# Optimization experiments

Hardware: AMD Instinct MI355X
Metric: run time of the kernel (lower is better)

## Reference

```python
import jax, jax.numpy as jnp
import numpy as np

GAMMA = 0.01
INFER_STEP = 5


def softor(x, axis, gamma=GAMMA):
    # gamma * logsumexp(x / gamma) along `axis`, rescaled by global max if it exceeds 1
    y = gamma * jax.nn.logsumexp(x / gamma, axis=axis)
    mx = jnp.max(y)
    return jnp.where(mx > 1.0, y / mx, y)


def setup_inputs() -> dict:
    key = jax.random.key(0)
    k1, k2, k3 = jax.random.split(key, 3)
    B, G, C, S, L, m = 32, 2048, 16, 8, 3, 16
    x = jax.random.uniform(k1, (B, G), dtype=jnp.float32)          # valuation vector in [0,1]
    W = jax.random.normal(k2, (m, C), dtype=jnp.float32)           # clause-assignment weights
    I = jax.random.randint(k3, (C, G, S, L), 0, G)                 # index tensor into atom axis
    return {"x": x, "W": W, "I": I}


def reference(x, W, I):
    # x: [B,G] valuations; W: [m,C]; I: [C,G,S,L] int indices into G
    def r(V):
        # all C clause functions at once: gather V along atom axis using I
        gathered = V[:, I]                      # [B,C,G,S,L]
        body = jnp.prod(gathered, axis=-1)      # conjunction over body literals -> [B,C,G,S]
        Cv = softor(body, axis=-1)              # softor over substitutions -> [B,C,G]
        Ws = jax.nn.softmax(W, axis=1)          # [m,C]
        H = jnp.einsum('mc,bcg->mbg', Ws, Cv)   # weighted clause mix -> [m,B,G]
        return softor(H, axis=0)                # softor over m heads -> [B,G]

    R = x
    for _ in range(INFER_STEP):
        R = softor(jnp.stack([R, r(R)], axis=1), axis=1)  # amalgamate old and new facts
    return R
```

## Files before the change

kernel.cpp:

```cpp
#include <hip/hip_runtime.h>

#define GAMMA 0.01f
#define B 32
#define G 2048
#define C 16
#define S 8
#define L 3
#define M 16
#define NBLK 256
#define NTHR 256

#define K_EXP 144.26950408889634f
#define K_LOG 0.006931471805599453f

#define SCOPE __HIP_MEMORY_SCOPE_AGENT

__device__ __forceinline__ unsigned ald(const unsigned* p) {
    return __hip_atomic_load(p, __ATOMIC_RELAXED, SCOPE);
}
__device__ __forceinline__ void ast(unsigned* p, unsigned v) {
    __hip_atomic_store(p, v, __ATOMIC_RELAXED, SCOPE);
}
__device__ __forceinline__ float aldf(const float* p) {
    return __hip_atomic_load(p, __ATOMIC_RELAXED, SCOPE);
}
__device__ __forceinline__ void astf(float* p, float v) {
    __hip_atomic_store(p, v, __ATOMIC_RELAXED, SCOPE);
}

__device__ __forceinline__ float waveMax(float v) {
#pragma unroll
    for (int off = 32; off > 0; off >>= 1)
        v = fmaxf(v, __shfl_xor(v, off, 64));
    return v;
}

__device__ __forceinline__ float blockMaxBcast(float v, float* scratch) {
    float wm = waveMax(v);
    __syncthreads();
    if ((threadIdx.x & 63) == 0) scratch[threadIdx.x >> 6] = wm;
    __syncthreads();
    return fmaxf(fmaxf(scratch[0], scratch[1]), fmaxf(scratch[2], scratch[3]));
}

__device__ __forceinline__ void blockMaxOut(float v, float* scratch, float* dst) {
    float wm = waveMax(v);
    __syncthreads();
    if ((threadIdx.x & 63) == 0) scratch[threadIdx.x >> 6] = wm;
    __syncthreads();
    if (threadIdx.x == 0)
        astf(&dst[blockIdx.x],
             fmaxf(fmaxf(scratch[0], scratch[1]), fmaxf(scratch[2], scratch[3])));
}

__device__ __forceinline__ void gridBarrier(unsigned* slots, unsigned* gen,
                                            unsigned* rgen, int bid, unsigned ep) {
    __syncthreads();
    const int t = threadIdx.x;
    if (bid == 0) {
        if (t > 0) {
            int guard = 0;
            while (ald(&slots[t * 32]) < ep && ++guard < (1 << 17)) {}
        }
        __syncthreads();
        if (t == 0) {
            asm volatile("s_waitcnt vmcnt(0) lgkmcnt(0)" ::: "memory");
            ast(gen, ep);
        }
    } else {
        if (t == 0) {
            asm volatile("s_waitcnt vmcnt(0) lgkmcnt(0)" ::: "memory");
            ast(&slots[bid * 32], ep);
            int guard = 0;
            if (bid <= 16) {
                while (ald(gen) < ep && ++guard < (1 << 17)) {}
                ast(&rgen[bid * 32], ep);
            } else {
                const int r = 1 + (bid & 15);
                while (ald(&rgen[r * 32]) < ep && ++guard < (1 << 17)) {}
            }
        }
        __syncthreads();
    }
}

extern "C" __global__ __launch_bounds__(256) void kmain(
    const float* __restrict__ x, const float* __restrict__ W,
    const int* __restrict__ I,
    unsigned* __restrict__ slots, unsigned* __restrict__ gen,
    unsigned* __restrict__ rgen, unsigned* __restrict__ Ipk,
    float* __restrict__ Pm1, float* __restrict__ Pm2, float* __restrict__ Pm3,
    float* __restrict__ Ry, float* __restrict__ out)
{
    __shared__ __align__(16) float Vrow[G];
    __shared__ float WsL[C * M];
    __shared__ float scratch[4];

    const int t = threadIdx.x;
    const int bid = blockIdx.x;
    const int b = bid & 31;
    const int gt = bid >> 5;
    const int g = (gt << 8) + t;
    const int i = b * G + g;
    unsigned ep = 0;

    {
        const int m = t >> 4, c = t & 15;
        float rmax = -INFINITY;
#pragma unroll
        for (int j = 0; j < C; j++) rmax = fmaxf(rmax, W[m * C + j]);
        float rsum = 0.f;
#pragma unroll
        for (int j = 0; j < C; j++) rsum += __expf(W[m * C + j] - rmax);
        WsL[c * M + m] = __expf(W[m * C + c] - rmax) / rsum;
    }
    {
        const int tid = bid * NTHR + t;
        if (tid < C * G) {
            const int4* ip4 = (const int4*)(I + (size_t)tid * 24);
            int idx[24];
#pragma unroll
            for (int j = 0; j < 6; j++) {
                int4 v = ip4[j];
                idx[4 * j + 0] = v.x; idx[4 * j + 1] = v.y;
                idx[4 * j + 2] = v.z; idx[4 * j + 3] = v.w;
            }
            unsigned* dst = Ipk + (size_t)tid * 12;
#pragma unroll
            for (int j = 0; j < 12; j++)
                ast(&dst[j],
                    ((unsigned)idx[2 * j] << 2) | ((unsigned)idx[2 * j + 1] << 18));
        }
    }
    gridBarrier(slots, gen, rgen, bid, ++ep);

    float ry = 0.f;
    for (int it = 0; it < 5; it++) {
        float s = 1.0f;
        if (it > 0) {
            float m3 = blockMaxBcast(aldf(&Pm3[t]), scratch);
            s = (m3 > 1.0f) ? 1.0f / m3 : 1.0f;
        }
        if (it == 0) {
            const float4* V4 = (const float4*)(x + (size_t)b * G);
            float4* Vr4 = (float4*)Vrow;
#pragma unroll
            for (int j = 0; j < 2; j++) Vr4[t + j * 256] = V4[t + j * 256];
        } else {
            const float* src = Ry + (size_t)b * G;
#pragma unroll
            for (int j = 0; j < 8; j++) {
                const int gg = t + j * 256;
                Vrow[gg] = s * aldf(&src[gg]);
            }
        }
        __syncthreads();

        float h[M];
#pragma unroll
        for (int m = 0; m < M; m++) h[m] = 0.f;
        float ymax = -INFINITY;
        const char* vb = (const char*)Vrow;

#pragma unroll 4
        for (int c = 0; c < C; c++) {
            const uint4* ip = (const uint4*)(Ipk + ((size_t)c * G + g) * 12);
            uint4 u0 = ip[0], u1 = ip[1], u2 = ip[2];
            unsigned w[12] = {u0.x, u0.y, u0.z, u0.w, u1.x, u1.y,
                              u1.z, u1.w, u2.x, u2.y, u2.z, u2.w};
            float vv[24];
#pragma unroll
            for (int q = 0; q < 12; q++) {
                vv[2 * q]     = *(const float*)(vb + (w[q] & 0xffffu));
                vv[2 * q + 1] = *(const float*)(vb + (w[q] >> 16));
            }
            float body[S];
#pragma unroll
            for (int ss = 0; ss < S; ss++)
                body[ss] = vv[ss * 3] * vv[ss * 3 + 1] * vv[ss * 3 + 2];
            float bm = body[0];
#pragma unroll
            for (int ss = 1; ss < S; ss++) bm = fmaxf(bm, body[ss]);
            float sum = 0.f;
#pragma unroll
            for (int ss = 0; ss < S; ss++)
                sum += exp2f((body[ss] - bm) * K_EXP);
            float y = fmaf(K_LOG, log2f(sum), bm);
            ymax = fmaxf(ymax, y);
#pragma unroll
            for (int m = 0; m < M; m++)
                h[m] = fmaf(WsL[c * M + m], y, h[m]);
        }
        blockMaxOut(ymax, scratch, Pm1);
        gridBarrier(slots, gen, rgen, bid, ++ep);

        float hy;
        {
            float m1 = blockMaxBcast(aldf(&Pm1[t]), scratch);
            float s1 = (m1 > 1.0f) ? 1.0f / m1 : 1.0f;
            float hv[M];
            float hm = -INFINITY;
#pragma unroll
            for (int m = 0; m < M; m++) {
                hv[m] = s1 * h[m];
                hm = fmaxf(hm, hv[m]);
            }
            float sum = 0.f;
#pragma unroll
            for (int m = 0; m < M; m++) sum += exp2f((hv[m] - hm) * K_EXP);
            hy = fmaf(K_LOG, log2f(sum), hm);
            blockMaxOut(hy, scratch, Pm2);
        }
        gridBarrier(slots, gen, rgen, bid, ++ep);

        {
            float m2 = blockMaxBcast(aldf(&Pm2[t]), scratch);
            float s2 = (m2 > 1.0f) ? 1.0f / m2 : 1.0f;
            float Rv = Vrow[g];
            float rv = s2 * hy;
            float a = fmaxf(Rv, rv), d = fminf(Rv, rv);
            ry = fmaf(K_LOG, log2f(1.0f + exp2f((d - a) * K_EXP)), a);
            astf(&Ry[i], ry);
            blockMaxOut(ry, scratch, Pm3);
        }
        gridBarrier(slots, gen, rgen, bid, ++ep);
    }

    float m3 = blockMaxBcast(aldf(&Pm3[t]), scratch);
    float sf = (m3 > 1.0f) ? 1.0f / m3 : 1.0f;
    out[i] = sf * ry;
}

extern "C" void kernel_launch(void* const* d_in, const int* in_sizes, int n_in,
                              void* d_out, int out_size, void* d_ws, size_t ws_size,
                              hipStream_t stream) {
    const float* x = (const float*)d_in[0];
    const float* W = (const float*)d_in[1];
    const int*   I = (const int*)d_in[2];
    float* out = (float*)d_out;

    unsigned* slots = (unsigned*)d_ws;
    unsigned* gen   = slots + NBLK * 32;
    unsigned* rgen  = gen + 32;
    float* Pm1 = (float*)(rgen + 17 * 32);
    float* Pm2 = Pm1 + NBLK;
    float* Pm3 = Pm2 + NBLK;
    float* Ry  = Pm3 + NBLK;
    unsigned* Ipk = (unsigned*)(Ry + (size_t)B * G);

    hipMemsetAsync(slots, 0, (NBLK * 32 + 32 + 17 * 32) * sizeof(unsigned),
                   stream);

    kmain<<<dim3(NBLK), dim3(NTHR), 0, stream>>>(
        x, W, I, slots, gen, rgen, Ipk, Pm1, Pm2, Pm3, Ry, out);
}
```

Before: 174.4 us.

## Fuse grid barrier with max reduction via epoch-tagged 64-bit slots

Replaces the hierarchical grid barrier (master block plus relay generation flags) and the separate partial-max arrays with one all-to-all scheme. Each block publishes a 64-bit packet holding its epoch and its block max. Every thread then polls one block's slot until the epoch matches, and a block max-reduce over the polled values gives the global max. This removes the extra barrier hops and separate loads per reduction, but has all 256 blocks polling 256 slots at once, which puts more traffic on the memory system.

```diff
diff --git a/kernel.cpp b/kernel.cpp
--- a/kernel.cpp
+++ b/kernel.cpp
@@ -9,15 +9,13 @@
 #define M 16
 #define NBLK 256
 #define NTHR 256
+#define SLOT_STRIDE 16
 
 #define K_EXP 144.26950408889634f
 #define K_LOG 0.006931471805599453f
 
 #define SCOPE __HIP_MEMORY_SCOPE_AGENT
 
-__device__ __forceinline__ unsigned ald(const unsigned* p) {
-    return __hip_atomic_load(p, __ATOMIC_RELAXED, SCOPE);
-}
 __device__ __forceinline__ void ast(unsigned* p, unsigned v) {
     __hip_atomic_store(p, v, __ATOMIC_RELAXED, SCOPE);
 }
@@ -43,53 +41,36 @@
     return fmaxf(fmaxf(scratch[0], scratch[1]), fmaxf(scratch[2], scratch[3]));
 }
 
-__device__ __forceinline__ void blockMaxOut(float v, float* scratch, float* dst) {
+__device__ __forceinline__ float gridMaxBarrier(unsigned long long* slot,
+                                                unsigned ep, float v,
+                                                float* scratch) {
     float wm = waveMax(v);
     __syncthreads();
     if ((threadIdx.x & 63) == 0) scratch[threadIdx.x >> 6] = wm;
     __syncthreads();
-    if (threadIdx.x == 0)
-        astf(&dst[blockIdx.x],
-             fmaxf(fmaxf(scratch[0], scratch[1]), fmaxf(scratch[2], scratch[3])));
-}
-
-__device__ __forceinline__ void gridBarrier(unsigned* slots, unsigned* gen,
-                                            unsigned* rgen, int bid, unsigned ep) {
-    __syncthreads();
-    const int t = threadIdx.x;
-    if (bid == 0) {
-        if (t > 0) {
-            int guard = 0;
-            while (ald(&slots[t * 32]) < ep && ++guard < (1 << 17)) {}
-        }
-        __syncthreads();
-        if (t == 0) {
-            asm volatile("s_waitcnt vmcnt(0) lgkmcnt(0)" ::: "memory");
-            ast(gen, ep);
-        }
-    } else {
-        if (t == 0) {
-            asm volatile("s_waitcnt vmcnt(0) lgkmcnt(0)" ::: "memory");
-            ast(&slots[bid * 32], ep);
-            int guard = 0;
-            if (bid <= 16) {
-                while (ald(gen) < ep && ++guard < (1 << 17)) {}
-                ast(&rgen[bid * 32], ep);
-            } else {
-                const int r = 1 + (bid & 15);
-                while (ald(&rgen[r * 32]) < ep && ++guard < (1 << 17)) {}
-            }
-        }
-        __syncthreads();
-    }
+    if (threadIdx.x == 0) {
+        float bm = fmaxf(fmaxf(scratch[0], scratch[1]),
+                         fmaxf(scratch[2], scratch[3]));
+        unsigned long long pkt = ((unsigned long long)ep << 32) |
+                                 (unsigned long long)__float_as_uint(bm);
+        asm volatile("s_waitcnt vmcnt(0) lgkmcnt(0)" ::: "memory");
+        __hip_atomic_store(&slot[(size_t)blockIdx.x * SLOT_STRIDE], pkt,
+                           __ATOMIC_RELAXED, SCOPE);
+    }
+    unsigned long long got;
+    int guard = 0;
+    do {
+        got = __hip_atomic_load(&slot[(size_t)threadIdx.x * SLOT_STRIDE],
+                                __ATOMIC_RELAXED, SCOPE);
+    } while ((unsigned)(got >> 32) < ep && ++guard < (1 << 17));
+    return blockMaxBcast(__uint_as_float((unsigned)got), scratch);
 }
 
 extern "C" __global__ __launch_bounds__(256) void kmain(
     const float* __restrict__ x, const float* __restrict__ W,
     const int* __restrict__ I,
-    unsigned* __restrict__ slots, unsigned* __restrict__ gen,
-    unsigned* __restrict__ rgen, unsigned* __restrict__ Ipk,
-    float* __restrict__ Pm1, float* __restrict__ Pm2, float* __restrict__ Pm3,
+    unsigned long long* __restrict__ slotA, unsigned long long* __restrict__ slotB,
+    unsigned long long* __restrict__ slotC, unsigned* __restrict__ Ipk,
     float* __restrict__ Ry, float* __restrict__ out)
 {
     __shared__ __align__(16) float Vrow[G];
@@ -102,7 +83,6 @@
     const int gt = bid >> 5;
     const int g = (gt << 8) + t;
     const int i = b * G + g;
-    unsigned ep = 0;
 
     {
         const int m = t >> 4, c = t & 15;
@@ -132,15 +112,13 @@
                     ((unsigned)idx[2 * j] << 2) | ((unsigned)idx[2 * j + 1] << 18));
         }
     }
-    gridBarrier(slots, gen, rgen, bid, ++ep);
+    float m3 = gridMaxBarrier(slotC, 1, -INFINITY, scratch);
 
     float ry = 0.f;
     for (int it = 0; it < 5; it++) {
         float s = 1.0f;
-        if (it > 0) {
-            float m3 = blockMaxBcast(aldf(&Pm3[t]), scratch);
+        if (it > 0)
             s = (m3 > 1.0f) ? 1.0f / m3 : 1.0f;
-        }
         if (it == 0) {
             const float4* V4 = (const float4*)(x + (size_t)b * G);
             float4* Vr4 = (float4*)Vrow;
@@ -191,12 +169,10 @@
             for (int m = 0; m < M; m++)
                 h[m] = fmaf(WsL[c * M + m], y, h[m]);
         }
-        blockMaxOut(ymax, scratch, Pm1);
-        gridBarrier(slots, gen, rgen, bid, ++ep);
+        float m1 = gridMaxBarrier(slotA, it + 1, ymax, scratch);
 
         float hy;
         {
-            float m1 = blockMaxBcast(aldf(&Pm1[t]), scratch);
             float s1 = (m1 > 1.0f) ? 1.0f / m1 : 1.0f;
             float hv[M];
             float hm = -INFINITY;
@@ -209,24 +185,20 @@
 #pragma unroll
             for (int m = 0; m < M; m++) sum += exp2f((hv[m] - hm) * K_EXP);
             hy = fmaf(K_LOG, log2f(sum), hm);
-            blockMaxOut(hy, scratch, Pm2);
-        }
-        gridBarrier(slots, gen, rgen, bid, ++ep);
+        }
+        float m2 = gridMaxBarrier(slotB, it + 1, hy, scratch);
 
         {
-            float m2 = blockMaxBcast(aldf(&Pm2[t]), scratch);
             float s2 = (m2 > 1.0f) ? 1.0f / m2 : 1.0f;
             float Rv = Vrow[g];
             float rv = s2 * hy;
             float a = fmaxf(Rv, rv), d = fminf(Rv, rv);
             ry = fmaf(K_LOG, log2f(1.0f + exp2f((d - a) * K_EXP)), a);
             astf(&Ry[i], ry);
-            blockMaxOut(ry, scratch, Pm3);
-        }
-        gridBarrier(slots, gen, rgen, bid, ++ep);
-    }
-
-    float m3 = blockMaxBcast(aldf(&Pm3[t]), scratch);
+        }
+        m3 = gridMaxBarrier(slotC, it + 2, ry, scratch);
+    }
+
     float sf = (m3 > 1.0f) ? 1.0f / m3 : 1.0f;
     out[i] = sf * ry;
 }
@@ -239,18 +211,15 @@
     const int*   I = (const int*)d_in[2];
     float* out = (float*)d_out;
 
-    unsigned* slots = (unsigned*)d_ws;
-    unsigned* gen   = slots + NBLK * 32;
-    unsigned* rgen  = gen + 32;
-    float* Pm1 = (float*)(rgen + 17 * 32);
-    float* Pm2 = Pm1 + NBLK;
-    float* Pm3 = Pm2 + NBLK;
-    float* Ry  = Pm3 + NBLK;
+    unsigned long long* slotA = (unsigned long long*)d_ws;
+    unsigned long long* slotB = slotA + NBLK * SLOT_STRIDE;
+    unsigned long long* slotC = slotB + NBLK * SLOT_STRIDE;
+    float* Ry = (float*)(slotC + NBLK * SLOT_STRIDE);
     unsigned* Ipk = (unsigned*)(Ry + (size_t)B * G);
 
-    hipMemsetAsync(slots, 0, (NBLK * 32 + 32 + 17 * 32) * sizeof(unsigned),
+    hipMemsetAsync(slotA, 0, 3 * NBLK * SLOT_STRIDE * sizeof(unsigned long long),
                    stream);
 
     kmain<<<dim3(NBLK), dim3(NTHR), 0, stream>>>(
-        x, W, I, slots, gen, rgen, Ipk, Pm1, Pm2, Pm3, Ry, out);
-}
+        x, W, I, slotA, slotB, slotC, Ipk, Ry, out);
+}
```

Result: faster. 166.6 us (-4.5%).
